# Performance work log

Hardware: AMD Instinct MI355X
Metric: run time of the kernel (lower is better)

## Reference

```python
import jax, jax.numpy as jnp
import numpy as np

B, V, C, H, W, D = 2, 3, 8, 128, 160, 64


def bilinear_sample(feat, grid):
    """feat: [B,C,H,W]; grid: [B,N,2] normalized to [-1,1], align_corners=True,
    padding_mode='zeros' (matches F.grid_sample). Returns [B,C,N]."""
    b, c, h, w = feat.shape
    ix = (grid[..., 0] + 1.0) * 0.5 * (w - 1)  # [B,N]
    iy = (grid[..., 1] + 1.0) * 0.5 * (h - 1)
    x0 = jnp.floor(ix)
    y0 = jnp.floor(iy)
    wx1 = ix - x0
    wy1 = iy - y0
    flat = feat.reshape(b, c, h * w)

    def corner(xi, yi, wgt):
        valid = (xi >= 0) & (xi <= w - 1) & (yi >= 0) & (yi <= h - 1)
        xc = jnp.clip(xi, 0, w - 1).astype(jnp.int32)
        yc = jnp.clip(yi, 0, h - 1).astype(jnp.int32)
        idx = yc * w + xc  # [B,N]
        vals = jnp.take_along_axis(flat, jnp.broadcast_to(idx[:, None, :], (b, c, idx.shape[1])), axis=2)
        return vals * (wgt * valid.astype(feat.dtype))[:, None, :]

    out = (corner(x0, y0, (1 - wx1) * (1 - wy1))
           + corner(x0 + 1, y0, wx1 * (1 - wy1))
           + corner(x0, y0 + 1, (1 - wx1) * wy1)
           + corner(x0 + 1, y0 + 1, wx1 * wy1))
    return out


def homo_warping(src_feat, proj_mat, depth_values):
    """src_feat [B,C,H,W], proj_mat [B,3,4], depth_values [B,D,H,W].
    Returns warped volume [B,C,D,H,W] and normalized grid [B,D,H,W,2]."""
    b, c, h, w = src_feat.shape
    d = depth_values.shape[1]
    R = proj_mat[:, :, :3]
    T = proj_mat[:, :, 3:]  # [B,3,1]
    ys, xs = jnp.meshgrid(jnp.arange(h, dtype=src_feat.dtype),
                          jnp.arange(w, dtype=src_feat.dtype), indexing='ij')
    ref = jnp.stack([xs.ravel(), ys.ravel(), jnp.ones(h * w, src_feat.dtype)], 0)  # [3,HW]
    Rp = jnp.einsum('bij,jp->bip', R, ref)  # [B,3,HW]
    dv = depth_values.reshape(b, d, h * w)
    src = Rp[:, :, None, :] + T[:, :, :, None] / dv[:, None, :, :]  # [B,3,D,HW]
    xy = src[:, :2] / src[:, 2:3]
    gx = xy[:, 0] / ((w - 1) / 2.0) - 1.0
    gy = xy[:, 1] / ((h - 1) / 2.0) - 1.0
    grid = jnp.stack([gx, gy], axis=-1)  # [B,D,HW,2]
    warped = bilinear_sample(src_feat, grid.reshape(b, d * h * w, 2)).reshape(b, c, d, h, w)
    return warped, grid.reshape(b, d, h, w, 2)


def setup_inputs() -> dict:
    key = jax.random.key(0)
    k1, k2, k3, k4, k5 = jax.random.split(key, 5)
    features = jax.random.normal(k1, (V, B, C, H, W), dtype=jnp.float32)
    # near-identity projective maps so warps land mostly in-bounds
    eye = jnp.broadcast_to(jnp.eye(3, dtype=jnp.float32), (B, V, 3, 3))
    Rm = eye + 0.01 * jax.random.normal(k2, (B, V, 3, 3), dtype=jnp.float32)
    Tm = 2.0 * jax.random.normal(k3, (B, V, 3, 1), dtype=jnp.float32)
    proj_matrices = jnp.concatenate([Rm, Tm], axis=-1)  # [B,V,3,4]
    base = jnp.linspace(2.0, 10.0, D, dtype=jnp.float32)[None, :, None, None]
    depth_values = base + 0.1 * jax.random.uniform(k4, (B, D, H, W), dtype=jnp.float32)
    reg_weight = jax.random.normal(k5, (C,), dtype=jnp.float32)
    return {"features": features, "proj_matrices": proj_matrices,
            "depth_values": depth_values, "reg_weight": reg_weight,
            "num_depth": D}


def reference(features, proj_matrices, depth_values, reg_weight, num_depth):
    v = features.shape[0]
    ref_feat = features[0]
    b, c, h, w = ref_feat.shape
    d = num_depth
    ref_volume = jnp.broadcast_to(ref_feat[:, :, None], (b, c, d, h, w))
    volume_sum = ref_volume
    volume_sq_sum = ref_volume ** 2
    in_masks = jnp.ones((b, 1, d, h, w), dtype=ref_feat.dtype)
    for i in range(1, v):  # fixed small number of source views
        warped, grid = homo_warping(features[i], proj_matrices[:, i], depth_values)
        m = (grid > -1.0) & (grid < 1.0)
        in_masks = in_masks + (m[..., 0] & m[..., 1]).astype(ref_feat.dtype)[:, None]
        volume_sum = volume_sum + warped
        volume_sq_sum = volume_sq_sum + warped ** 2
    count = 1.0 / in_masks
    volume_feat = volume_sq_sum * count - (volume_sum * count) ** 2  # [B,C,D,H,W]
    # stand-in cost regularization: channel reduction -> [B,D,H,W]
    cost = jnp.einsum('bcdhw,c->bdhw', volume_feat, reg_weight)
    prob_volume = jax.nn.softmax(cost, axis=1)
    depth = jnp.sum(prob_volume * depth_values, axis=1)  # [B,H,W]
    return depth
```

## Files before the change

kernel.cpp:

```cpp
#include <hip/hip_runtime.h>
#include <math.h>

#define BB 2
#define VV 3
#define CC 8
#define HH 128
#define WW 160
#define DD 64
constexpr int HW = HH * WW;
constexpr int NPIX = BB * HW;
constexpr int LANES_PER_PIX = 16;
constexpr int DEPTHS_PER_LANE = DD / LANES_PER_PIX;
constexpr int PIX_PER_WAVE = 64 / LANES_PER_PIX;

__global__ __launch_bounds__(256)
void transpose_feats(const float* __restrict__ feats, float* __restrict__ ft)
{
    const int t = blockIdx.x * blockDim.x + threadIdx.x;
    if (t >= VV * BB * HW) return;
    const int vb = t / HW;
    const int hw = t - vb * HW;
    const float* src = feats + (size_t)vb * CC * HW + hw;
    float* dst = ft + (size_t)vb * HW * CC + (size_t)hw * CC;
    float4 lo, hi;
    lo.x = src[0 * HW]; lo.y = src[1 * HW]; lo.z = src[2 * HW]; lo.w = src[3 * HW];
    hi.x = src[4 * HW]; hi.y = src[5 * HW]; hi.z = src[6 * HW]; hi.w = src[7 * HW];
    ((float4*)dst)[0] = lo;
    ((float4*)dst)[1] = hi;
}

__global__ __launch_bounds__(256)
void depthnet_fused(const float* __restrict__ ft,
                    const float* __restrict__ proj,
                    const float* __restrict__ depthv,
                    const float* __restrict__ regw,
                    float* __restrict__ out)
{
    const int t     = blockIdx.x * blockDim.x + threadIdx.x;
    const int lane  = threadIdx.x & 63;
    const int waveg = t >> 6;
    const int pl    = lane & (PIX_PER_WAVE - 1);
    const int chunk = lane >> 2;
    const int pixel = waveg * PIX_PER_WAVE + pl;

    const int b  = (pixel >= HW) ? 1 : 0;
    const int hw = pixel - b * HW;
    const int h  = hw / WW;
    const int w  = hw - h * WW;

    const float* f0 = ft + ((size_t)b * HW + hw) * CC;
    float rf[CC];
    {
        float4 lo = ((const float4*)f0)[0];
        float4 hi = ((const float4*)f0)[1];
        rf[0] = lo.x; rf[1] = lo.y; rf[2] = lo.z; rf[3] = lo.w;
        rf[4] = hi.x; rf[5] = hi.y; rf[6] = hi.z; rf[7] = hi.w;
    }

    float Rp[2][3], Tv[2][3];
    const float xf = (float)w, yf = (float)h;
#pragma unroll
    for (int v = 0; v < 2; ++v) {
        const float* M = proj + ((size_t)b * VV + (v + 1)) * 12;
#pragma unroll
        for (int i = 0; i < 3; ++i) {
            Rp[v][i] = M[i * 4 + 0] * xf + M[i * 4 + 1] * yf + M[i * 4 + 2];
            Tv[v][i] = M[i * 4 + 3];
        }
    }

    const float* fsrc0 = ft + ((size_t)(1 * BB + b)) * HW * CC;
    const float* fsrc1 = ft + ((size_t)(2 * BB + b)) * HW * CC;

    float m = -INFINITY, l = 0.f, s = 0.f;

    const float* dvp = depthv + (size_t)b * DD * HW + hw;
    const int d0 = chunk * DEPTHS_PER_LANE;

    for (int dd = 0; dd < DEPTHS_PER_LANE; ++dd) {
        const int d = d0 + dd;
        const float dv = dvp[(size_t)d * HW];
        const float inv_dv = 1.0f / dv;

        float sum[CC], sq[CC];
#pragma unroll
        for (int c = 0; c < CC; ++c) { sum[c] = rf[c]; sq[c] = rf[c] * rf[c]; }
        float nmask = 1.0f;

#pragma unroll
        for (int v = 0; v < 2; ++v) {
            const float* fb = (v == 0) ? fsrc0 : fsrc1;
            const float sx = Rp[v][0] + Tv[v][0] * inv_dv;
            const float sy = Rp[v][1] + Tv[v][1] * inv_dv;
            const float sz = Rp[v][2] + Tv[v][2] * inv_dv;
            const float xi = sx / sz;
            const float yi = sy / sz;
            const float gx = xi / ((WW - 1) * 0.5f) - 1.0f;
            const float gy = yi / ((HH - 1) * 0.5f) - 1.0f;
            nmask += ((gx > -1.0f) && (gx < 1.0f) && (gy > -1.0f) && (gy < 1.0f)) ? 1.0f : 0.0f;
            const float ix = (gx + 1.0f) * 0.5f * (float)(WW - 1);
            const float iy = (gy + 1.0f) * 0.5f * (float)(HH - 1);
            const float x0f = floorf(ix), y0f = floorf(iy);
            const float wx1 = ix - x0f, wy1 = iy - y0f;
            const float wx0 = 1.f - wx1, wy0 = 1.f - wy1;
            const float x1f = x0f + 1.f, y1f = y0f + 1.f;
            const bool vx0 = (x0f >= 0.f) && (x0f <= (float)(WW - 1));
            const bool vx1 = (x1f >= 0.f) && (x1f <= (float)(WW - 1));
            const bool vy0 = (y0f >= 0.f) && (y0f <= (float)(HH - 1));
            const bool vy1 = (y1f >= 0.f) && (y1f <= (float)(HH - 1));
            const float w00 = wx0 * wy0 * ((vx0 && vy0) ? 1.f : 0.f);
            const float w01 = wx1 * wy0 * ((vx1 && vy0) ? 1.f : 0.f);
            const float w10 = wx0 * wy1 * ((vx0 && vy1) ? 1.f : 0.f);
            const float w11 = wx1 * wy1 * ((vx1 && vy1) ? 1.f : 0.f);
            const int x0c = (int)fminf(fmaxf(x0f, 0.f), (float)(WW - 1));
            const int x1c = (int)fminf(fmaxf(x1f, 0.f), (float)(WW - 1));
            const int y0c = (int)fminf(fmaxf(y0f, 0.f), (float)(HH - 1));
            const int y1c = (int)fminf(fmaxf(y1f, 0.f), (float)(HH - 1));
            const int i00 = (y0c * WW + x0c) * CC;
            const int i01 = (y0c * WW + x1c) * CC;
            const int i10 = (y1c * WW + x0c) * CC;
            const int i11 = (y1c * WW + x1c) * CC;

            float val[CC];
#pragma unroll
            for (int c = 0; c < CC; ++c) val[c] = 0.f;

            {
                float4 lo = *(const float4*)(fb + i00);
                float4 hi = *(const float4*)(fb + i00 + 4);
                val[0] += lo.x * w00; val[1] += lo.y * w00; val[2] += lo.z * w00; val[3] += lo.w * w00;
                val[4] += hi.x * w00; val[5] += hi.y * w00; val[6] += hi.z * w00; val[7] += hi.w * w00;
            }
            {
                float4 lo = *(const float4*)(fb + i01);
                float4 hi = *(const float4*)(fb + i01 + 4);
                val[0] += lo.x * w01; val[1] += lo.y * w01; val[2] += lo.z * w01; val[3] += lo.w * w01;
                val[4] += hi.x * w01; val[5] += hi.y * w01; val[6] += hi.z * w01; val[7] += hi.w * w01;
            }
            {
                float4 lo = *(const float4*)(fb + i10);
                float4 hi = *(const float4*)(fb + i10 + 4);
                val[0] += lo.x * w10; val[1] += lo.y * w10; val[2] += lo.z * w10; val[3] += lo.w * w10;
                val[4] += hi.x * w10; val[5] += hi.y * w10; val[6] += hi.z * w10; val[7] += hi.w * w10;
            }
            {
                float4 lo = *(const float4*)(fb + i11);
                float4 hi = *(const float4*)(fb + i11 + 4);
                val[0] += lo.x * w11; val[1] += lo.y * w11; val[2] += lo.z * w11; val[3] += lo.w * w11;
                val[4] += hi.x * w11; val[5] += hi.y * w11; val[6] += hi.z * w11; val[7] += hi.w * w11;
            }

#pragma unroll
            for (int c = 0; c < CC; ++c) {
                sum[c] += val[c];
                sq[c]  += val[c] * val[c];
            }
        }

        const float cnt = 1.0f / nmask;
        float cost = 0.f;
#pragma unroll
        for (int c = 0; c < CC; ++c) {
            const float mean = sum[c] * cnt;
            const float vf = sq[c] * cnt - mean * mean;
            cost += vf * regw[c];
        }

        const float M = fmaxf(m, cost);
        const float e_old = __expf(m - M);
        const float e_new = __expf(cost - M);
        l = l * e_old + e_new;
        s = s * e_old + e_new * dv;
        m = M;
    }

#pragma unroll
    for (int off = 4; off < 64; off <<= 1) {
        const float m2 = __shfl_xor(m, off, 64);
        const float l2 = __shfl_xor(l, off, 64);
        const float s2 = __shfl_xor(s, off, 64);
        const float M  = fmaxf(m, m2);
        const float e1 = __expf(m - M);
        const float e2 = __expf(m2 - M);
        l = l * e1 + l2 * e2;
        s = s * e1 + s2 * e2;
        m = M;
    }

    if (chunk == 0) out[pixel] = s / l;
}

extern "C" void kernel_launch(void* const* d_in, const int* in_sizes, int n_in,
                              void* d_out, int out_size, void* d_ws, size_t ws_size,
                              hipStream_t stream) {
    const float* feats  = (const float*)d_in[0];
    const float* proj   = (const float*)d_in[1];
    const float* depthv = (const float*)d_in[2];
    const float* regw   = (const float*)d_in[3];
    float* out = (float*)d_out;
    float* ft  = (float*)d_ws;

    {
        const int n = VV * BB * HW;
        const int block = 256;
        const int grid = (n + block - 1) / block;
        hipLaunchKernelGGL(transpose_feats, dim3(grid), dim3(block), 0, stream,
                           feats, ft);
    }
    {
        const int total_threads = NPIX * LANES_PER_PIX;
        const int block = 256;
        const int grid = (total_threads + block - 1) / block;
        hipLaunchKernelGGL(depthnet_fused, dim3(grid), dim3(block), 0, stream,
                           ft, proj, depthv, regw, out);
    }
}
```

Before: 106.5 us.

## Remap pixels to 32-lane groups with 8 depth chunks and LDS softmax merge

```diff
diff --git a/kernel.cpp b/kernel.cpp
--- a/kernel.cpp
+++ b/kernel.cpp
@@ -9,9 +9,9 @@
 #define DD 64
 constexpr int HW = HH * WW;
 constexpr int NPIX = BB * HW;
-constexpr int LANES_PER_PIX = 16;
-constexpr int DEPTHS_PER_LANE = DD / LANES_PER_PIX;
-constexpr int PIX_PER_WAVE = 64 / LANES_PER_PIX;
+constexpr int PX_PER_BLOCK = 32;
+constexpr int CHUNKS = 8;
+constexpr int DEPTHS_PER_CHUNK = DD / CHUNKS;
 
 __global__ __launch_bounds__(256)
 void transpose_feats(const float* __restrict__ feats, float* __restrict__ ft)
@@ -29,19 +29,24 @@
     ((float4*)dst)[1] = hi;
 }
 
-__global__ __launch_bounds__(256)
+__global__ __launch_bounds__(256, 4)
 void depthnet_fused(const float* __restrict__ ft,
                     const float* __restrict__ proj,
                     const float* __restrict__ depthv,
                     const float* __restrict__ regw,
                     float* __restrict__ out)
 {
-    const int t     = blockIdx.x * blockDim.x + threadIdx.x;
-    const int lane  = threadIdx.x & 63;
-    const int waveg = t >> 6;
-    const int pl    = lane & (PIX_PER_WAVE - 1);
-    const int chunk = lane >> 2;
-    const int pixel = waveg * PIX_PER_WAVE + pl;
+    __shared__ float sm_m[PX_PER_BLOCK * 4];
+    __shared__ float sm_l[PX_PER_BLOCK * 4];
+    __shared__ float sm_s[PX_PER_BLOCK * 4];
+
+    const int tid   = threadIdx.x;
+    const int lane  = tid & 63;
+    const int wave  = tid >> 6;
+    const int px    = lane & 31;
+    const int sub   = lane >> 5;
+    const int chunk = wave * 2 + sub;
+    const int pixel = blockIdx.x * PX_PER_BLOCK + px;
 
     const int b  = (pixel >= HW) ? 1 : 0;
     const int hw = pixel - b * HW;
@@ -49,13 +54,15 @@
     const int w  = hw - h * WW;
 
     const float* f0 = ft + ((size_t)b * HW + hw) * CC;
-    float rf[CC];
+    float rf[CC], rf2[CC];
     {
         float4 lo = ((const float4*)f0)[0];
         float4 hi = ((const float4*)f0)[1];
         rf[0] = lo.x; rf[1] = lo.y; rf[2] = lo.z; rf[3] = lo.w;
         rf[4] = hi.x; rf[5] = hi.y; rf[6] = hi.z; rf[7] = hi.w;
     }
+#pragma unroll
+    for (int c = 0; c < CC; ++c) rf2[c] = rf[c] * rf[c];
 
     float Rp[2][3], Tv[2][3];
     const float xf = (float)w, yf = (float)h;
@@ -75,16 +82,17 @@
     float m = -INFINITY, l = 0.f, s = 0.f;
 
     const float* dvp = depthv + (size_t)b * DD * HW + hw;
-    const int d0 = chunk * DEPTHS_PER_LANE;
-
-    for (int dd = 0; dd < DEPTHS_PER_LANE; ++dd) {
+    const int d0 = chunk * DEPTHS_PER_CHUNK;
+
+#pragma unroll 4
+    for (int dd = 0; dd < DEPTHS_PER_CHUNK; ++dd) {
         const int d = d0 + dd;
         const float dv = dvp[(size_t)d * HW];
-        const float inv_dv = 1.0f / dv;
+        const float inv_dv = __builtin_amdgcn_rcpf(dv);
 
         float sum[CC], sq[CC];
 #pragma unroll
-        for (int c = 0; c < CC; ++c) { sum[c] = rf[c]; sq[c] = rf[c] * rf[c]; }
+        for (int c = 0; c < CC; ++c) { sum[c] = rf[c]; sq[c] = rf2[c]; }
         float nmask = 1.0f;
 
 #pragma unroll
@@ -93,13 +101,11 @@
             const float sx = Rp[v][0] + Tv[v][0] * inv_dv;
             const float sy = Rp[v][1] + Tv[v][1] * inv_dv;
             const float sz = Rp[v][2] + Tv[v][2] * inv_dv;
-            const float xi = sx / sz;
-            const float yi = sy / sz;
-            const float gx = xi / ((WW - 1) * 0.5f) - 1.0f;
-            const float gy = yi / ((HH - 1) * 0.5f) - 1.0f;
-            nmask += ((gx > -1.0f) && (gx < 1.0f) && (gy > -1.0f) && (gy < 1.0f)) ? 1.0f : 0.0f;
-            const float ix = (gx + 1.0f) * 0.5f * (float)(WW - 1);
-            const float iy = (gy + 1.0f) * 0.5f * (float)(HH - 1);
+            const float rsz = __builtin_amdgcn_rcpf(sz);
+            const float ix = sx * rsz;
+            const float iy = sy * rsz;
+            nmask += ((ix > 0.f) && (ix < (float)(WW - 1)) &&
+                      (iy > 0.f) && (iy < (float)(HH - 1))) ? 1.0f : 0.0f;
             const float x0f = floorf(ix), y0f = floorf(iy);
             const float wx1 = ix - x0f, wy1 = iy - y0f;
             const float wx0 = 1.f - wx1, wy0 = 1.f - wy1;
@@ -122,14 +128,11 @@
             const int i11 = (y1c * WW + x1c) * CC;
 
             float val[CC];
-#pragma unroll
-            for (int c = 0; c < CC; ++c) val[c] = 0.f;
-
             {
                 float4 lo = *(const float4*)(fb + i00);
                 float4 hi = *(const float4*)(fb + i00 + 4);
-                val[0] += lo.x * w00; val[1] += lo.y * w00; val[2] += lo.z * w00; val[3] += lo.w * w00;
-                val[4] += hi.x * w00; val[5] += hi.y * w00; val[6] += hi.z * w00; val[7] += hi.w * w00;
+                val[0] = lo.x * w00; val[1] = lo.y * w00; val[2] = lo.z * w00; val[3] = lo.w * w00;
+                val[4] = hi.x * w00; val[5] = hi.y * w00; val[6] = hi.z * w00; val[7] = hi.w * w00;
             }
             {
                 float4 lo = *(const float4*)(fb + i01);
@@ -157,14 +160,14 @@
             }
         }
 
-        const float cnt = 1.0f / nmask;
-        float cost = 0.f;
+        const float cnt = __builtin_amdgcn_rcpf(nmask);
+        float t1 = 0.f, t2 = 0.f;
 #pragma unroll
         for (int c = 0; c < CC; ++c) {
-            const float mean = sum[c] * cnt;
-            const float vf = sq[c] * cnt - mean * mean;
-            cost += vf * regw[c];
-        }
+            t1 += regw[c] * sq[c];
+            t2 += (regw[c] * sum[c]) * sum[c];
+        }
+        const float cost = cnt * t1 - (cnt * cnt) * t2;
 
         const float M = fmaxf(m, cost);
         const float e_old = __expf(m - M);
@@ -174,11 +177,10 @@
         m = M;
     }
 
-#pragma unroll
-    for (int off = 4; off < 64; off <<= 1) {
-        const float m2 = __shfl_xor(m, off, 64);
-        const float l2 = __shfl_xor(l, off, 64);
-        const float s2 = __shfl_xor(s, off, 64);
+    {
+        const float m2 = __shfl_xor(m, 32, 64);
+        const float l2 = __shfl_xor(l, 32, 64);
+        const float s2 = __shfl_xor(s, 32, 64);
         const float M  = fmaxf(m, m2);
         const float e1 = __expf(m - M);
         const float e2 = __expf(m2 - M);
@@ -187,7 +189,29 @@
         m = M;
     }
 
-    if (chunk == 0) out[pixel] = s / l;
+    if (lane < 32) {
+        sm_m[wave * PX_PER_BLOCK + px] = m;
+        sm_l[wave * PX_PER_BLOCK + px] = l;
+        sm_s[wave * PX_PER_BLOCK + px] = s;
+    }
+    __syncthreads();
+
+    if (tid < PX_PER_BLOCK) {
+        float M = sm_m[tid], L = sm_l[tid], S = sm_s[tid];
+#pragma unroll
+        for (int wv = 1; wv < 4; ++wv) {
+            const float m2 = sm_m[wv * PX_PER_BLOCK + tid];
+            const float l2 = sm_l[wv * PX_PER_BLOCK + tid];
+            const float s2 = sm_s[wv * PX_PER_BLOCK + tid];
+            const float Mn = fmaxf(M, m2);
+            const float e1 = __expf(M - Mn);
+            const float e2 = __expf(m2 - Mn);
+            L = L * e1 + l2 * e2;
+            S = S * e1 + s2 * e2;
+            M = Mn;
+        }
+        out[blockIdx.x * PX_PER_BLOCK + tid] = S / L;
+    }
 }
 
 extern "C" void kernel_launch(void* const* d_in, const int* in_sizes, int n_in,
@@ -208,10 +232,8 @@
                            feats, ft);
     }
     {
-        const int total_threads = NPIX * LANES_PER_PIX;
-        const int block = 256;
-        const int grid = (total_threads + block - 1) / block;
-        hipLaunchKernelGGL(depthnet_fused, dim3(grid), dim3(block), 0, stream,
+        const int grid = NPIX / PX_PER_BLOCK;
+        hipLaunchKernelGGL(depthnet_fused, dim3(grid), dim3(256), 0, stream,
                            ft, proj, depthv, regw, out);
     }
 }
```

Result: slower. 219.0 us (+105.7%).
